# Kernel optimization log

Measured on AMD Instinct MI355X. Metric: run time of the kernel, lower is better.

Reference implementation:

```python
import jax, jax.numpy as jnp
import numpy as np

N = 131072          # total nodes per batched graph side
E = 524288          # total edges per batched graph side (avg degree 4)
B = 4096            # number of graph pairs
NPG = 32            # nodes per graph
NEG_SLOPE = 0.2
LN_EPS = 1e-5


def setup_inputs() -> dict:
    key = jax.random.key(0)
    ks = jax.random.split(key, 40)
    rn = lambda k, s, sc=0.05: jax.random.normal(k, s, dtype=jnp.float32) * sc
    inp = {}
    inp["feat1"] = jax.random.normal(ks[0], (N, 6), dtype=jnp.float32)
    inp["feat2"] = jax.random.normal(ks[1], (N, 6), dtype=jnp.float32)
    inp["llm_emb"] = jax.random.normal(ks[2], (B, 1024), dtype=jnp.float32)
    inp["src1"] = jax.random.randint(ks[3], (E,), 0, N, dtype=jnp.int32)
    inp["dst1"] = jax.random.randint(ks[4], (E,), 0, N, dtype=jnp.int32)
    inp["src2"] = jax.random.randint(ks[5], (E,), 0, N, dtype=jnp.int32)
    inp["dst2"] = jax.random.randint(ks[6], (E,), 0, N, dtype=jnp.int32)
    inp["gid"] = (jnp.arange(N, dtype=jnp.int32) // NPG).astype(jnp.int32)
    # shared GAT weights (layer: W[in,H*Dh], attn_l[H,Dh], attn_r[H,Dh], bias[H*Dh])
    inp["W1"] = rn(ks[7], (6, 128));   inp["al1"] = rn(ks[8], (4, 32));  inp["ar1"] = rn(ks[9], (4, 32));  inp["b1"] = rn(ks[10], (128,))
    inp["W2"] = rn(ks[11], (128, 128)); inp["al2"] = rn(ks[12], (4, 32)); inp["ar2"] = rn(ks[13], (4, 32)); inp["b2"] = rn(ks[14], (128,))
    inp["W3"] = rn(ks[15], (128, 256)); inp["al3"] = rn(ks[16], (4, 64)); inp["ar3"] = rn(ks[17], (4, 64)); inp["b3"] = rn(ks[18], (256,))
    # fusion
    inp["Wpg"] = rn(ks[19], (512, 512)); inp["bpg"] = rn(ks[20], (512,))
    inp["Wpl"] = rn(ks[21], (1024, 512)); inp["bpl"] = rn(ks[22], (512,))
    inp["Wv"] = rn(ks[23], (512, 512));  inp["bv"] = rn(ks[24], (512,))
    inp["Wo"] = rn(ks[25], (512, 512));  inp["bo"] = rn(ks[26], (512,))
    inp["gamma"] = jnp.ones((512,), jnp.float32); inp["beta"] = jnp.zeros((512,), jnp.float32)
    # classifier
    inp["Wc1"] = rn(ks[27], (512, 256)); inp["bc1"] = rn(ks[28], (256,))
    inp["Wc2"] = rn(ks[29], (256, 1));   inp["bc2"] = rn(ks[30], (1,))
    return inp


def _gat(x, src, dst, W, al, ar, b):
    # DGL GATConv: e_ij = LeakyReLU(a_l.h_src + a_r.h_dst), softmax over edges per dst
    H, Dh = al.shape
    h = (x @ W).reshape(-1, H, Dh)                 # [N,H,Dh]
    el = jnp.sum(h * al, axis=-1)                  # [N,H]
    er = jnp.sum(h * ar, axis=-1)                  # [N,H]
    e = jax.nn.leaky_relu(el[src] + er[dst], NEG_SLOPE)   # [E,H]
    m = jax.ops.segment_max(e, dst, num_segments=N)
    a = jnp.exp(e - m[dst])
    s = jax.ops.segment_sum(a, dst, num_segments=N)
    alpha = a / jnp.where(s[dst] == 0, 1.0, s[dst])       # [E,H]
    out = jax.ops.segment_sum(alpha[:, :, None] * h[src], dst, num_segments=N)
    return out.reshape(-1, H * Dh) + b


def _gnn(x, src, dst, gid, W1, al1, ar1, b1, W2, al2, ar2, b2, W3, al3, ar3, b3):
    h = jax.nn.relu(_gat(x, src, dst, W1, al1, ar1, b1))
    h = jax.nn.relu(_gat(h, src, dst, W2, al2, ar2, b2))
    h = _gat(h, src, dst, W3, al3, ar3, b3)        # [N,256]
    sums = jax.ops.segment_sum(h, gid, num_segments=B)
    cnt = jax.ops.segment_sum(jnp.ones((h.shape[0], 1), h.dtype), gid, num_segments=B)
    return sums / cnt                               # [B,256] mean_nodes


def reference(feat1, feat2, llm_emb, src1, dst1, src2, dst2, gid,
              W1, al1, ar1, b1, W2, al2, ar2, b2, W3, al3, ar3, b3,
              Wpg, bpg, Wpl, bpl, Wv, bv, Wo, bo, gamma, beta,
              Wc1, bc1, Wc2, bc2):
    h1 = _gnn(feat1, src1, dst1, gid, W1, al1, ar1, b1, W2, al2, ar2, b2, W3, al3, ar3, b3)
    h2 = _gnn(feat2, src2, dst2, gid, W1, al1, ar1, b1, W2, al2, ar2, b2, W3, al3, ar3, b3)
    pair = jnp.concatenate([h1, h2], axis=1)        # [B,512]
    gp = pair @ Wpg + bpg                           # [B,512]
    lp = llm_emb @ Wpl + bpl                        # [B,512]
    # MHA with kv seq_len 1: softmax over a single key == 1 -> out = W_o(W_v gp)
    attn = (gp @ Wv + bv) @ Wo + bo
    x = attn + lp
    mu = jnp.mean(x, axis=-1, keepdims=True)
    var = jnp.mean((x - mu) ** 2, axis=-1, keepdims=True)
    fused = (x - mu) / jnp.sqrt(var + LN_EPS) * gamma + beta
    hcls = jax.nn.relu(fused @ Wc1 + bc1)
    return jax.nn.sigmoid(hcls @ Wc2 + bc2)         # [B,1]
```

## Files before the change

kernel.cpp:

```cpp
#include <hip/hip_runtime.h>
#include <hip/hip_fp8.h>

#define NN 131072
#define NE 524288
#define NB 4096
#define CAP 16
#define NEG_SLOPE 0.2f
#define LN_EPS 1e-5f
#define LOG2E 1.44269504088896f

#define NBKT 1024
#define NBLK1 256
#define CELL_CAP 24

typedef unsigned short bf16;
typedef __attribute__((ext_vector_type(8))) short short8;
typedef __attribute__((ext_vector_type(4))) float floatx4;
typedef __attribute__((ext_vector_type(2))) float floatx2;

#if __has_builtin(__builtin_amdgcn_exp2f)
#define EXP2(x) __builtin_amdgcn_exp2f(x)
#else
#define EXP2(x) exp2f(x)
#endif

__device__ __forceinline__ float bf2f(bf16 h) {
    return __uint_as_float((unsigned)h << 16);
}
__device__ __forceinline__ bf16 f2bf(float f) {
    unsigned u = __float_as_uint(f);
    unsigned r = (u + 0x7FFFu + ((u >> 16) & 1u)) >> 16;
    return (bf16)r;
}
__device__ __forceinline__ unsigned pkbf(float lo, float hi) {
    unsigned r;
    asm("v_cvt_pk_bf16_f32 %0, %1, %2" : "=v"(r) : "v"(lo), "v"(hi));
    return r;
}
__device__ __forceinline__ unsigned char ftofp8(float f) {
    return (unsigned char)(__builtin_amdgcn_cvt_pk_fp8_f32(f, f, 0, false) & 0xFF);
}
__device__ __forceinline__ float leaky(float x) {
    return fmaxf(x, 0.f) + NEG_SLOPE * fminf(x, 0.f);
}

__global__ __launch_bounds__(256) void part_edges_kernel(
        const int* __restrict__ s0, const int* __restrict__ d0,
        const int* __restrict__ s1, const int* __restrict__ d1,
        unsigned* __restrict__ cells, int* __restrict__ counts) {
    __shared__ int lcnt[NBKT];
    int blk = blockIdx.x, t = threadIdx.x;
    for (int i = t; i < NBKT; i += 256) lcnt[i] = 0;
    __syncthreads();
    int side = blk >= (NBLK1 / 2);
    const int4* dp = (const int4*)(side ? d1 : d0);
    const int4* sp = (const int4*)(side ? s1 : s0);
    int base4 = (blk - side * (NBLK1 / 2)) * 1024;
    int gbase = side * NN;
#pragma unroll
    for (int it = 0; it < 4; it++) {
        int e4 = base4 + it * 256 + t;
        int4 dd = dp[e4];
        int4 ss = sp[e4];
        int d[4] = {gbase + dd.x, gbase + dd.y, gbase + dd.z, gbase + dd.w};
        int s[4] = {gbase + ss.x, gbase + ss.y, gbase + ss.z, gbase + ss.w};
#pragma unroll
        for (int k = 0; k < 4; k++) {
            int b = d[k] >> 8;
            int r = atomicAdd(&lcnt[b], 1);
            if (r < CELL_CAP)
                cells[((size_t)b * NBLK1 + blk) * CELL_CAP + r] =
                    ((unsigned)s[k] << 8) | (unsigned)(d[k] & 255);
        }
    }
    __syncthreads();
    for (int i = t; i < NBKT; i += 256) {
        int c = lcnt[i];
        counts[i * NBLK1 + blk] = (c > CELL_CAP) ? CELL_CAP : c;
    }
}

__global__ __launch_bounds__(256) void build_slots_kernel(
        const unsigned* __restrict__ cells, const int* __restrict__ counts,
        int* __restrict__ deg, int* __restrict__ slots) {
    __shared__ int ldeg[256];
    __shared__ int lslot[256 * CAP];
    int b = blockIdx.x, t = threadIdx.x;
    ldeg[t] = 0;
    for (int i = t; i < 256 * CAP; i += 256) lslot[i] = 0;
    __syncthreads();
    int cnt = counts[b * NBLK1 + t];
    const unsigned* cp = cells + ((size_t)b * NBLK1 + t) * CELL_CAP;
    for (int i = 0; i < cnt; i++) {
        unsigned v = cp[i];
        int d = v & 255;
        int s = (int)(v >> 8);
        int p = atomicAdd(&ldeg[d], 1);
        if (p < CAP) lslot[d * CAP + p] = s;
    }
    __syncthreads();
    int node0 = b * 256;
    deg[node0 + t] = ldeg[t];
    for (int i = t; i < 256 * CAP; i += 256)
        slots[(size_t)node0 * CAP + i] = lslot[i];
}

#define PREP_TOTAL (16384 + 524288 + 131072 + 2048 + 2048 + 48 + 4096 + 131072)

__global__ void prep_all_kernel(const float* __restrict__ W2, const float* __restrict__ W3,
                                const float* __restrict__ Wpl, const float* __restrict__ Wc1,
                                const float* __restrict__ W1,
                                const float* __restrict__ al1, const float* __restrict__ ar1,
                                const float* __restrict__ al2, const float* __restrict__ ar2,
                                const float* __restrict__ al3, const float* __restrict__ ar3,
                                const float* __restrict__ b1v,
                                bf16* __restrict__ W2t, bf16* __restrict__ Wplt,
                                bf16* __restrict__ Wc1t,
                                bf16* __restrict__ Ff2, bf16* __restrict__ Ff3,
                                float* __restrict__ F1, bf16* __restrict__ W1f,
                                bf16* __restrict__ W3bdt) {
    int i = blockIdx.x * blockDim.x + threadIdx.x;
    if (i < 16384) {
        int c = i >> 7, k = i & 127;
        W2t[i] = f2bf(W2[k * 128 + c]);
        return;
    }
    i -= 16384;
    if (i < 524288) {
        int c = i >> 10, k = i & 1023;
        Wplt[i] = f2bf(Wpl[k * 512 + c]);
        return;
    }
    i -= 524288;
    if (i < 131072) {
        int c = i >> 9, k = i & 511;
        Wc1t[i] = f2bf(Wc1[k * 256 + c]);
        return;
    }
    i -= 131072;
    if (i < 2048) {
        int c = i >> 7, k = i & 127;
        float s = 0.f;
        if (c < 8) {
            const float* a = (c < 4) ? al2 : ar2;
            int hh = c & 3;
            for (int d = 0; d < 32; d++) s += W2[k * 128 + hh * 32 + d] * a[hh * 32 + d];
        }
        Ff2[i] = f2bf(s);
        return;
    }
    i -= 2048;
    if (i < 2048) {
        int c = i >> 7, k = i & 127;
        float s = 0.f;
        if (c < 8) {
            const float* a = (c < 4) ? al3 : ar3;
            int hh = c & 3;
            for (int d = 0; d < 64; d++) s += W3[k * 256 + hh * 64 + d] * a[hh * 64 + d];
        }
        Ff3[i] = f2bf(s);
        return;
    }
    i -= 2048;
    if (i < 48) {
        int k = i >> 3, c = i & 7;
        const float* a = (c < 4) ? al1 : ar1;
        int hh = c & 3;
        float s = 0.f;
        for (int d = 0; d < 32; d++) s += W1[k * 128 + hh * 32 + d] * a[hh * 32 + d];
        F1[k * 8 + c] = s * LOG2E;
        return;
    }
    i -= 48;
    if (i < 4096) {
        int c = i >> 5, k = i & 31;
        int h = c >> 5, d = k & 7;
        float v = 0.f;
        if ((k >> 3) == h) {
            if (d < 6) v = W1[d * 128 + c];
            else if (d == 6) v = b1v[c];
        }
        W1f[i] = f2bf(v);
        return;
    }
    i -= 4096;
    if (i < 131072) {
        int c = i >> 9, r = i & 511;
        int hr = r >> 7, k = r & 127;
        float v = (hr == (c >> 6)) ? W3[k * 256 + c] : 0.f;
        W3bdt[i] = f2bf(v);
    }
}

__global__ void f2bf_kernel(const float* __restrict__ x, bf16* __restrict__ y) {
    int i = blockIdx.x * blockDim.x + threadIdx.x;
    float4 v = ((const float4*)x)[i];
    ushort4 u;
    u.x = f2bf(v.x); u.y = f2bf(v.y); u.z = f2bf(v.z); u.w = f2bf(v.w);
    ((ushort4*)y)[i] = u;
}

__global__ void wt_kernel(const float* __restrict__ W, bf16* __restrict__ Wt, int K, int C) {
    int i = blockIdx.x * blockDim.x + threadIdx.x;
    if (i >= K * C) return;
    int c = i / K, k = i - c * K;
    Wt[i] = f2bf(W[(size_t)k * C + c]);
}


__global__ void featelr_kernel(const float* __restrict__ f0, const float* __restrict__ f1,
                               const float* __restrict__ F1, float* __restrict__ fpk,
                               float* __restrict__ el, float* __restrict__ er) {
    int n = blockIdx.x * blockDim.x + threadIdx.x;
    const float* x = (n < NN) ? (f0 + (size_t)n * 6) : (f1 + (size_t)(n - NN) * 6);
    float xv[6];
#pragma unroll
    for (int k = 0; k < 6; k++) xv[k] = x[k];
    float4* o = (float4*)(fpk + (size_t)n * 8);
    o[0] = make_float4(xv[0], xv[1], xv[2], xv[3]);
    o[1] = make_float4(xv[4], xv[5], 0.f, 0.f);
    float4 elv, erv;
    float* ep = (float*)&elv;
    float* rp = (float*)&erv;
#pragma unroll
    for (int c = 0; c < 4; c++) {
        float sl = 0.f, sr = 0.f;
#pragma unroll
        for (int k = 0; k < 6; k++) {
            sl += xv[k] * F1[k * 8 + c];
            sr += xv[k] * F1[k * 8 + c + 4];
        }
        ep[c] = sl;
        rp[c] = sr;
    }
    *(float4*)(el + (size_t)n * 4) = elv;
    *(float4*)(er + (size_t)n * 4) = erv;
}

__global__ __launch_bounds__(256) void agg1mfma_kernel(
        const float* __restrict__ fpk, const float* __restrict__ el,
        const float* __restrict__ er, const int* __restrict__ deg,
        const int* __restrict__ slots, const bf16* __restrict__ W1fg,
        bf16* __restrict__ xb) {
    __shared__ bf16 sW[128 * 40];
    __shared__ bf16 sagg[256 * 40];
    int t = threadIdx.x;
    if (t < 128) {
        const uint4* src = (const uint4*)(W1fg + t * 32);
        uint4* dstp = (uint4*)(sW + t * 40);
        dstp[0] = src[0]; dstp[1] = src[1]; dstp[2] = src[2]; dstp[3] = src[3];
    }

    int node = blockIdx.x * 256 + t;
    int dg = deg[node];
    dg = (dg > CAP) ? CAP : dg;
    float4 er4 = *(const float4*)(er + (size_t)node * 4);
    const int* sp = slots + (size_t)node * CAP;
    float a0[4], a1[4], a2[4], a3[4], a4[4], a5[4], ss[4];
#pragma unroll
    for (int h = 0; h < 4; h++) {
        a0[h] = a1[h] = a2[h] = a3[h] = a4[h] = a5[h] = ss[h] = 0.f;
    }
    for (int p = 0; p < dg; p += 4) {
        int4 s4 = *(const int4*)(sp + p);
        int sarr[4] = {s4.x, s4.y, s4.z, s4.w};
#pragma unroll
        for (int k = 0; k < 4; k++) {
            bool vld = (p + k) < dg;
            int g = vld ? sarr[k] : s4.x;
            float4 e4 = *(const float4*)(el + (size_t)g * 4);
            float4 xa = *(const float4*)(fpk + (size_t)g * 8);
            float4 xc = *(const float4*)(fpk + (size_t)g * 8 + 4);
            float eh[4] = {e4.x, e4.y, e4.z, e4.w};
            float rh[4] = {er4.x, er4.y, er4.z, er4.w};
#pragma unroll
            for (int h = 0; h < 4; h++) {
                float z = eh[h] + rh[h];
                float w = EXP2(fmaxf(z, 0.f) + NEG_SLOPE * fminf(z, 0.f));
                w = vld ? w : 0.f;
                ss[h] += w;
                a0[h] += w * xa.x; a1[h] += w * xa.y; a2[h] += w * xa.z;
                a3[h] += w * xa.w; a4[h] += w * xc.x; a5[h] += w * xc.y;
            }
        }
    }
#pragma unroll
    for (int h = 0; h < 4; h++) {
        float rs = (dg > 0) ? 1.f / ss[h] : 0.f;
        uint4 o;
        o.x = pkbf(a0[h] * rs, a1[h] * rs);
        o.y = pkbf(a2[h] * rs, a3[h] * rs);
        o.z = pkbf(a4[h] * rs, a5[h] * rs);
        o.w = 0x00003F80u;
        *(uint4*)(sagg + t * 40 + h * 8) = o;
    }
    __syncthreads();

    int wave = t >> 6, lane = t & 63;
    int mlane = lane & 15, quad = lane >> 4;
    short8 af[8];
#pragma unroll
    for (int j = 0; j < 8; j++)
        af[j] = *(const short8*)(sW + (j * 16 + mlane) * 40 + quad * 8);
    floatx4 z4 = (floatx4){0.f, 0.f, 0.f, 0.f};
#pragma unroll
    for (int nt = 0; nt < 4; nt++) {
        int lrow = wave * 64 + nt * 16 + mlane;
        short8 bfr = *(const short8*)(sagg + lrow * 40 + quad * 8);
        floatx4 c[8];
#pragma unroll
        for (int j = 0; j < 8; j++)
            c[j] = __builtin_amdgcn_mfma_f32_16x16x32_bf16(af[j], bfr, z4, 0, 0, 0);
        bf16* op = xb + (size_t)(blockIdx.x * 256 + lrow) * 128 + quad * 4;
#pragma unroll
        for (int j = 0; j < 8; j++) {
            uint2 o;
            o.x = pkbf(fmaxf(c[j][0], 0.f), fmaxf(c[j][1], 0.f));
            o.y = pkbf(fmaxf(c[j][2], 0.f), fmaxf(c[j][3], 0.f));
            *(uint2*)(op + j * 16) = o;
        }
    }
}


__device__ __forceinline__ void softmax_phaseA(const float* __restrict__ el,
                                               const float* __restrict__ er,
                                               const int* __restrict__ slots,
                                               int wid, int dg, int lane,
                                               float* alpha_out, int* src_out) {
    int e = lane & 15, h = lane >> 4;
    int sA = slots[(size_t)wid * CAP + e];
    int sAc = (e < dg) ? sA : 0;
    float erh = er[wid * 4 + h];
    float elv = el[sAc * 4 + h];
    float w = (e < dg) ? __expf(leaky(elv + erh)) : 0.f;
    float ssum = w;
    ssum += __shfl_xor(ssum, 1, 64);
    ssum += __shfl_xor(ssum, 2, 64);
    ssum += __shfl_xor(ssum, 4, 64);
    ssum += __shfl_xor(ssum, 8, 64);
    *alpha_out = (dg > 0) ? w * (1.f / ssum) : 0.f;
    *src_out = sAc;
}

__global__ void agg2_kernel(const unsigned char* __restrict__ h8, const float* __restrict__ el,
                            const float* __restrict__ er, const int* __restrict__ deg,
                            const int* __restrict__ slots, const float* __restrict__ bias,
                            unsigned char* __restrict__ out) {
    int t = blockIdx.x * blockDim.x + threadIdx.x;
    int wid = t >> 5;
    int gl = threadIdx.x & 31;
    int dg = deg[wid];
    dg = (dg > CAP) ? CAP : dg;
    int head = gl >> 3;
    int fbase = gl * 4;
    float erh = er[wid * 4 + head];
    const int* sp = slots + (size_t)wid * CAP;
    float a0 = 0.f, a1 = 0.f, a2 = 0.f, a3 = 0.f, ssum = 0.f;

    for (int p = 0; p < dg; p += 4) {
        int4 s4 = *(const int4*)(sp + p);
        int s[4]; bool v[4];
        s[0] = s4.x; v[0] = true;
        v[1] = p + 1 < dg; s[1] = v[1] ? s4.y : s4.x;
        v[2] = p + 2 < dg; s[2] = v[2] ? s4.z : s4.x;
        v[3] = p + 3 < dg; s[3] = v[3] ? s4.w : s4.x;
        float elv[4]; unsigned u1[4];
#pragma unroll
        for (int k = 0; k < 4; k++) {
            elv[k] = el[s[k] * 4 + head];
            u1[k] = *(const unsigned*)(h8 + (size_t)s[k] * 128 + fbase);
        }
#pragma unroll
        for (int k = 0; k < 4; k++) {
            float w = v[k] ? __expf(leaky(elv[k] + erh)) : 0.f;
            ssum += w;
            floatx2 lo = __builtin_amdgcn_cvt_pk_f32_fp8((int)u1[k], false);
            floatx2 hi = __builtin_amdgcn_cvt_pk_f32_fp8((int)u1[k], true);
            a0 += w * lo[0]; a1 += w * lo[1];
            a2 += w * hi[0]; a3 += w * hi[1];
        }
    }
    float rs = (dg > 0) ? 1.f / ssum : 0.f;
    float4 bbv = *(const float4*)(bias + fbase);
    float v0 = fmaxf(a0 * rs + bbv.x, 0.f), v1 = fmaxf(a1 * rs + bbv.y, 0.f);
    float v2 = fmaxf(a2 * rs + bbv.z, 0.f), v3 = fmaxf(a3 * rs + bbv.w, 0.f);
    unsigned w8 = (unsigned)__builtin_amdgcn_cvt_pk_fp8_f32(v0, v1, 0, false);
    w8 = (unsigned)__builtin_amdgcn_cvt_pk_fp8_f32(v2, v3, (int)w8, true);
    *(unsigned*)(out + (size_t)wid * 128 + fbase) = w8;
}

__global__ __launch_bounds__(256) void elr3_kernel(const unsigned char* __restrict__ x8,
                                                   const bf16* __restrict__ Ff3,
                                                   float* __restrict__ el,
                                                   float* __restrict__ er) {
    int wave = threadIdx.x >> 6, lane = threadIdx.x & 63;
    int mlane = lane & 15, quad = lane >> 4;
    int node0 = blockIdx.x * 64 + wave * 16;
    floatx4 acc = (floatx4){0.f, 0.f, 0.f, 0.f};
#pragma unroll
    for (int kb = 0; kb < 4; kb++) {
        short8 bfr = *(const short8*)(Ff3 + mlane * 128 + kb * 32 + quad * 8);
        uint2 u8 = *(const uint2*)(x8 + (size_t)(node0 + mlane) * 128 + kb * 32 + quad * 8);
        floatx2 f01 = __builtin_amdgcn_cvt_pk_f32_fp8((int)u8.x, false);
        floatx2 f23 = __builtin_amdgcn_cvt_pk_f32_fp8((int)u8.x, true);
        floatx2 f45 = __builtin_amdgcn_cvt_pk_f32_fp8((int)u8.y, false);
        floatx2 f67 = __builtin_amdgcn_cvt_pk_f32_fp8((int)u8.y, true);
        short8 af;
        unsigned* ap = (unsigned*)&af;
        ap[0] = pkbf(f01[0], f01[1]); ap[1] = pkbf(f23[0], f23[1]);
        ap[2] = pkbf(f45[0], f45[1]); ap[3] = pkbf(f67[0], f67[1]);
        acc = __builtin_amdgcn_mfma_f32_16x16x32_bf16(af, bfr, acc, 0, 0, 0);
    }
    if (mlane < 8) {
        float* dst = (mlane < 4) ? el : er;
        int h = mlane & 3;
#pragma unroll
        for (int r = 0; r < 4; r++) {
            int node = node0 + quad * 4 + r;
            dst[node * 4 + h] = acc[r];
        }
    }
}

__global__ void agg3pool_kernel(const unsigned char* __restrict__ x8,
                                const float* __restrict__ el, const float* __restrict__ er,
                                const int* __restrict__ deg, const int* __restrict__ slots,
                                bf16* __restrict__ poolagg) {
    __shared__ float red[4][4][128];
    __shared__ float salpha[4][136][4];
    __shared__ int   ssrc[4][136];
    int side = blockIdx.x >> 12;
    int b = blockIdx.x & 4095;
    int nodebase = side * NN + b * 32;
    int grp = threadIdx.x >> 6, lane = threadIdx.x & 63;
    int e = lane & 15, h = lane >> 4;
    int esl = lane >> 5;
    int ch4 = (lane & 31) * 4;

    int off = 0;
    for (int nn = 0; nn < 8; nn++) {
        int wid = nodebase + grp * 8 + nn;
        int dg = deg[wid];
        dg = (dg > CAP) ? CAP : dg;
        float alpha; int sAc;
        softmax_phaseA(el, er, slots, wid, dg, lane, &alpha, &sAc);
        if (e < dg) {
            salpha[grp][off + e][h] = alpha;
            if (h == 0) ssrc[grp][off + e] = sAc;
        }
        off += dg;
    }
    int padded = (off + 7) & ~7;
    if (lane < padded - off) {
        int j = off + lane;
        *(float4*)&salpha[grp][j][0] = make_float4(0.f, 0.f, 0.f, 0.f);
        ssrc[grp][j] = 0;
    }

    floatx2 acc[4][2];
#pragma unroll
    for (int hh = 0; hh < 4; hh++) {
        acc[hh][0] = (floatx2){0.f, 0.f};
        acc[hh][1] = (floatx2){0.f, 0.f};
    }
    for (int j = 0; j < padded; j += 8) {
        int sc[4]; float4 av[4]; unsigned u[4];
#pragma unroll
        for (int k = 0; k < 4; k++) {
            int je = j + 2 * k + esl;
            sc[k] = ssrc[grp][je];
            av[k] = *(const float4*)&salpha[grp][je][0];
        }
#pragma unroll
        for (int k = 0; k < 4; k++)
            u[k] = *(const unsigned*)(x8 + (size_t)sc[k] * 128 + ch4);
#pragma unroll
        for (int k = 0; k < 4; k++) {
            floatx2 lo = __builtin_amdgcn_cvt_pk_f32_fp8((int)u[k], false);
            floatx2 hi = __builtin_amdgcn_cvt_pk_f32_fp8((int)u[k], true);
            float aa[4] = {av[k].x, av[k].y, av[k].z, av[k].w};
#pragma unroll
            for (int hh = 0; hh < 4; hh++) {
                floatx2 a2 = (floatx2){aa[hh], aa[hh]};
                acc[hh][0] += a2 * lo;
                acc[hh][1] += a2 * hi;
            }
        }
    }
#pragma unroll
    for (int hh = 0; hh < 4; hh++)
#pragma unroll
        for (int jj = 0; jj < 2; jj++) {
            acc[hh][jj][0] += __shfl_xor(acc[hh][jj][0], 32, 64);
            acc[hh][jj][1] += __shfl_xor(acc[hh][jj][1], 32, 64);
        }
    if (lane < 32) {
#pragma unroll
        for (int hh = 0; hh < 4; hh++)
            *(float4*)&red[grp][hh][ch4] =
                make_float4(acc[hh][0][0], acc[hh][0][1], acc[hh][1][0], acc[hh][1][1]);
    }
    __syncthreads();
    int t = threadIdx.x;
    int hlo = t >> 7, c = t & 127;
    float s0 = 0.f, s1 = 0.f;
#pragma unroll
    for (int g = 0; g < 4; g++) {
        s0 += red[g][hlo][c];
        s1 += red[g][2 + hlo][c];
    }
    const float inv = 1.0f / 32.0f;
    size_t gbase = (size_t)(b * 2 + side) * 512;
    poolagg[gbase + t] = f2bf(s0 * inv);
    poolagg[gbase + t + 256] = f2bf(s1 * inv);
}

template <bool FOLD, bool OUT8, bool PAIR>
__global__ __launch_bounds__(256) void mgemm_kernel(const bf16* __restrict__ A,
                                                    const bf16* __restrict__ Wt,
                                                    const float* __restrict__ bias,
                                                    void* __restrict__ out,
                                                    int K, int C, int relu,
                                                    const bf16* __restrict__ Ff,
                                                    float* __restrict__ el,
                                                    float* __restrict__ er) {
    __shared__ short As[128 * 48];
    __shared__ short Bs[128 * 48];
    int t = threadIdx.x;
    int wave = t >> 6, lane = t & 63;
    int wm = (wave >> 1) * 64, wn = (wave & 1) * 64;
    int bm = blockIdx.x * 128, bn = blockIdx.y * 128;
    int m_lane = lane & 15, quad = lane >> 4;
    bool dofold = FOLD && (blockIdx.y == 0) && (wn == 0);

    floatx4 acc[4][4];
#pragma unroll
    for (int i = 0; i < 4; i++)
#pragma unroll
        for (int j = 0; j < 4; j++) acc[i][j] = (floatx4){0.f, 0.f, 0.f, 0.f};
    floatx4 facc[4];
    if (FOLD) {
#pragma unroll
        for (int i = 0; i < 4; i++) facc[i] = (floatx4){0.f, 0.f, 0.f, 0.f};
    }

    int lrow = t >> 2, lq = t & 3;
    for (int k0 = 0; k0 < K; k0 += 32) {
        __syncthreads();
#pragma unroll
        for (int pass = 0; pass < 2; pass++) {
            int row = lrow + pass * 64;
            *(short8*)&As[row * 48 + lq * 8] =
                *(const short8*)(A + (size_t)(bm + row) * K + k0 + lq * 8);
            *(short8*)&Bs[row * 48 + lq * 8] =
                *(const short8*)(Wt + (size_t)(bn + row) * K + k0 + lq * 8);
        }
        __syncthreads();
        short8 af[4], bf[4];
#pragma unroll
        for (int i = 0; i < 4; i++)
            af[i] = *(const short8*)&As[(wm + i * 16 + m_lane) * 48 + quad * 8];
#pragma unroll
        for (int j = 0; j < 4; j++)
            bf[j] = *(const short8*)&Bs[(wn + j * 16 + m_lane) * 48 + quad * 8];
        if (dofold) {
            short8 fbv = *(const short8*)(Ff + m_lane * K + k0 + quad * 8);
#pragma unroll
            for (int i = 0; i < 4; i++)
                facc[i] = __builtin_amdgcn_mfma_f32_16x16x32_bf16(af[i], fbv, facc[i], 0, 0, 0);
        }
#pragma unroll
        for (int i = 0; i < 4; i++)
#pragma unroll
            for (int j = 0; j < 4; j++)
                acc[i][j] = __builtin_amdgcn_mfma_f32_16x16x32_bf16(af[i], bf[j], acc[i][j], 0, 0, 0);
    }

#pragma unroll
    for (int i = 0; i < 4; i++) {
#pragma unroll
        for (int j = 0; j < 4; j++) {
            int gc = bn + wn + j * 16 + m_lane;
            float bbv = bias ? bias[gc] : 0.f;
#pragma unroll
            for (int r = 0; r < 4; r++) {
                int gr = bm + wm + i * 16 + quad * 4 + r;
                float v = acc[i][j][r] + bbv;
                if (relu) v = fmaxf(v, 0.f);
                if (OUT8)      ((unsigned char*)out)[(size_t)gr * C + gc] = ftofp8(v);
                else if (PAIR) ((bf16*)out)[(size_t)(gr >> 1) * 512 + (gr & 1) * 256 + gc] = f2bf(v);
                else           ((bf16*)out)[(size_t)gr * C + gc] = f2bf(v);
            }
        }
    }
    if (dofold && m_lane < 8) {
        float* dst = (m_lane < 4) ? el : er;
        int hh = m_lane & 3;
#pragma unroll
        for (int i = 0; i < 4; i++)
#pragma unroll
            for (int r = 0; r < 4; r++) {
                int gr = bm + wm + i * 16 + quad * 4 + r;
                dst[gr * 4 + hh] = facc[i][r];
            }
    }
}

__global__ __launch_bounds__(256) void fgemm512_kernel(const float* __restrict__ A,
                                                       const float* __restrict__ B,
                                                       float* __restrict__ C) {
    const int BK = 16;
    __shared__ float As[BK][68];
    __shared__ float Bs[BK][68];
    int t = threadIdx.x;
    int bm = blockIdx.x * 64, bn = blockIdx.y * 64;
    int tm0 = (t & 15) * 4, tn0 = (t >> 4) * 4;
    float acc[4][4] = {};
    int la_m = t >> 2, la_k = (t & 3) * 4;
    int lb_k = t >> 4, lb_c = (t & 15) * 4;

    for (int k0 = 0; k0 < 512; k0 += BK) {
        float4 a4 = *(const float4*)(A + (size_t)(bm + la_m) * 512 + k0 + la_k);
        float4 b4 = *(const float4*)(B + (size_t)(k0 + lb_k) * 512 + bn + lb_c);
        As[la_k + 0][la_m] = a4.x; As[la_k + 1][la_m] = a4.y;
        As[la_k + 2][la_m] = a4.z; As[la_k + 3][la_m] = a4.w;
        *(float4*)&Bs[lb_k][lb_c] = b4;
        __syncthreads();
#pragma unroll
        for (int k = 0; k < BK; k++) {
            float4 av = *(const float4*)&As[k][tm0];
            float4 bv = *(const float4*)&Bs[k][tn0];
            acc[0][0] += av.x * bv.x; acc[0][1] += av.x * bv.y; acc[0][2] += av.x * bv.z; acc[0][3] += av.x * bv.w;
            acc[1][0] += av.y * bv.x; acc[1][1] += av.y * bv.y; acc[1][2] += av.y * bv.z; acc[1][3] += av.y * bv.w;
            acc[2][0] += av.z * bv.x; acc[2][1] += av.z * bv.y; acc[2][2] += av.z * bv.z; acc[2][3] += av.z * bv.w;
            acc[3][0] += av.w * bv.x; acc[3][1] += av.w * bv.y; acc[3][2] += av.w * bv.z; acc[3][3] += av.w * bv.w;
        }
        __syncthreads();
    }
#pragma unroll
    for (int i = 0; i < 4; i++) {
        float4 o = make_float4(acc[i][0], acc[i][1], acc[i][2], acc[i][3]);
        *(float4*)(C + (size_t)(bm + tm0 + i) * 512 + bn + tn0) = o;
    }
}

__global__ void biasstep_kernel(const float* __restrict__ vin, const float* __restrict__ M,
                                const float* __restrict__ badd, float* __restrict__ vout) {
    int c = blockIdx.x * blockDim.x + threadIdx.x;
    float s = 0.f;
    for (int k = 0; k < 512; k++) s += vin[k] * M[(size_t)k * 512 + c];
    vout[c] = s + badd[c];
}


__global__ void ln_kernel(const bf16* __restrict__ attn, const bf16* __restrict__ lp,
                          const float* __restrict__ gamma, const float* __restrict__ beta,
                          bf16* __restrict__ out) {
    __shared__ float red[256];
    int b = blockIdx.x, t = threadIdx.x;
    size_t base = (size_t)b * 512;
    float x0 = bf2f(attn[base + t]) + bf2f(lp[base + t]);
    float x1 = bf2f(attn[base + 256 + t]) + bf2f(lp[base + 256 + t]);
    red[t] = x0 + x1; __syncthreads();
    for (int off = 128; off > 0; off >>= 1) { if (t < off) red[t] += red[t + off]; __syncthreads(); }
    float mu = red[0] * (1.0f / 512.0f);
    __syncthreads();
    float d0 = x0 - mu, d1 = x1 - mu;
    red[t] = d0 * d0 + d1 * d1; __syncthreads();
    for (int off = 128; off > 0; off >>= 1) { if (t < off) red[t] += red[t + off]; __syncthreads(); }
    float rstd = rsqrtf(red[0] * (1.0f / 512.0f) + LN_EPS);
    out[base + t]       = f2bf(d0 * rstd * gamma[t] + beta[t]);
    out[base + 256 + t] = f2bf(d1 * rstd * gamma[256 + t] + beta[256 + t]);
}

__global__ void cls2_kernel(const bf16* __restrict__ hc, const float* __restrict__ Wc2,
                            const float* __restrict__ bc2, float* __restrict__ out) {
    int wid = (blockIdx.x * blockDim.x + threadIdx.x) >> 6;
    int lane = threadIdx.x & 63;
    if (wid >= NB) return;
    float s = 0.f;
#pragma unroll
    for (int j = 0; j < 4; j++) {
        int k = lane + 64 * j;
        s += bf2f(hc[(size_t)wid * 256 + k]) * Wc2[k];
    }
    for (int off = 32; off > 0; off >>= 1) s += __shfl_down(s, off);
    if (lane == 0) {
        float v = s + bc2[0];
        out[wid] = 1.0f / (1.0f + __expf(-v));
    }
}


static inline size_t alup(size_t x) { return (x + 255) & ~(size_t)255; }

extern "C" void kernel_launch(void* const* d_in, const int* in_sizes, int n_in,
                              void* d_out, int out_size, void* d_ws, size_t ws_size,
                              hipStream_t stream) {
    const float* feat0 = (const float*)d_in[0];
    const float* feat1 = (const float*)d_in[1];
    const float* llm = (const float*)d_in[2];
    const int* srcs[2] = {(const int*)d_in[3], (const int*)d_in[5]};
    const int* dsts[2] = {(const int*)d_in[4], (const int*)d_in[6]};
    const float* W1 = (const float*)d_in[8];
    const float* al[3] = {(const float*)d_in[9],  (const float*)d_in[13], (const float*)d_in[17]};
    const float* ar[3] = {(const float*)d_in[10], (const float*)d_in[14], (const float*)d_in[18]};
    const float* bb[3] = {(const float*)d_in[11], (const float*)d_in[15], (const float*)d_in[19]};
    const float* W2 = (const float*)d_in[12];
    const float* W3 = (const float*)d_in[16];
    const float* Wpg = (const float*)d_in[20]; const float* bpg = (const float*)d_in[21];
    const float* Wpl = (const float*)d_in[22]; const float* bpl = (const float*)d_in[23];
    const float* Wv  = (const float*)d_in[24]; const float* bv  = (const float*)d_in[25];
    const float* Wo  = (const float*)d_in[26]; const float* bo  = (const float*)d_in[27];
    const float* gamma = (const float*)d_in[28]; const float* beta = (const float*)d_in[29];
    const float* Wc1 = (const float*)d_in[30]; const float* bc1 = (const float*)d_in[31];
    const float* Wc2 = (const float*)d_in[32]; const float* bc2 = (const float*)d_in[33];
    float* outp = (float*)d_out;

    const size_t N2 = (size_t)2 * NN;

    char* p = (char*)d_ws;
    auto take = [&](size_t bytes) { char* r = p; p += alup(bytes); return r; };
    bf16*  xb     = (bf16*)take(N2 * 128 * 2);
    char*  regB   = (char*)take(N2 * 256);
    float* el     = (float*)take(N2 * 4 * 4);
    float* er     = (float*)take(N2 * 4 * 4);
    int*   deg    = (int*)take(N2 * 4);
    int*   slots  = (int*)take(N2 * CAP * 4);
    bf16*  pair   = (bf16*)take((size_t)NB * 512 * 2);
    bf16*  llm_bf = (bf16*)take((size_t)NB * 1024 * 2);
    bf16*  W2t  = (bf16*)take(128 * 128 * 2);
    bf16*  Wplt = (bf16*)take(1024 * 512 * 2);
    bf16*  Wc1t = (bf16*)take(512 * 256 * 2);
    bf16*  Wcot = (bf16*)take(512 * 512 * 2);
    bf16*  W3bdt = (bf16*)take(256 * 512 * 2);
    float* F1   = (float*)take(6 * 8 * 4);
    bf16*  Ff2  = (bf16*)take(16 * 128 * 2);
    bf16*  Ff3  = (bf16*)take(16 * 128 * 2);
    bf16*  W1fg = (bf16*)take(128 * 32 * 2);
    float* c1   = (float*)take(512 * 512 * 4);
    float* c2   = (float*)take(512 * 512 * 4);
    float* bias1 = (float*)take(512 * 4);
    float* bco   = (float*)take(512 * 4);
    unsigned char* x8 = (unsigned char*)xb;
    unsigned* cells = (unsigned*)regB;
    int* counts = (int*)(regB + (size_t)NBKT * NBLK1 * CELL_CAP * 4);
    float* fpk          = (float*)regB;
    unsigned char* hb2  = (unsigned char*)regB;
    bf16* poolagg = (bf16*)(regB + 32 * 1024 * 1024);
    bf16* fbb   = (bf16*)regB;
    bf16* lp    = fbb + (size_t)0 * NB * 512;
    bf16* attn  = fbb + (size_t)1 * NB * 512;
    bf16* fused = fbb + (size_t)2 * NB * 512;
    bf16* hc    = fbb + (size_t)3 * NB * 512;
    (void)ws_size; (void)n_in; (void)in_sizes; (void)out_size;

    auto mgemm = [&](const bf16* A, const bf16* Wt, const float* bias, bf16* o,
                     int M, int K, int C, int relu) {
        dim3 g(M / 128, C / 128);
        mgemm_kernel<false, false, false><<<g, 256, 0, stream>>>(A, Wt, bias, o, K, C, relu,
                                                                 nullptr, nullptr, nullptr);
    };

    part_edges_kernel<<<NBLK1, 256, 0, stream>>>(srcs[0], dsts[0], srcs[1], dsts[1],
                                                 cells, counts);
    build_slots_kernel<<<NBKT, 256, 0, stream>>>(cells, counts, deg, slots);

    prep_all_kernel<<<(PREP_TOTAL + 255) / 256, 256, 0, stream>>>(
        W2, W3, Wpl, Wc1, W1, al[0], ar[0], al[1], ar[1], al[2], ar[2], bb[0],
        W2t, Wplt, Wc1t, Ff2, Ff3, F1, W1fg, W3bdt);
    f2bf_kernel<<<NB * 1024 / 4 / 256, 256, 0, stream>>>(llm, llm_bf);
    {
        dim3 g8(8, 8);
        fgemm512_kernel<<<g8, 256, 0, stream>>>(Wpg, Wv, c1);
        fgemm512_kernel<<<g8, 256, 0, stream>>>(c1, Wo, c2);
        wt_kernel<<<(512 * 512 + 255) / 256, 256, 0, stream>>>(c2, Wcot, 512, 512);
        biasstep_kernel<<<2, 256, 0, stream>>>(bpg, Wv, bv, bias1);
        biasstep_kernel<<<2, 256, 0, stream>>>(bias1, Wo, bo, bco);
    }

    featelr_kernel<<<2 * NN / 256, 256, 0, stream>>>(feat0, feat1, F1, fpk, el, er);
    agg1mfma_kernel<<<2 * NN / 256, 256, 0, stream>>>(fpk, el, er, deg, slots, W1fg, xb);
    {
        dim3 g(2 * NN / 128, 1);
        mgemm_kernel<true, true, false><<<g, 256, 0, stream>>>(xb, W2t, nullptr, hb2,
                                                               128, 128, 0, Ff2, el, er);
    }
    agg2_kernel<<<2 * NN * 32 / 256, 256, 0, stream>>>(hb2, el, er, deg, slots, bb[1], x8);
    elr3_kernel<<<2 * NN / 64, 256, 0, stream>>>(x8, Ff3, el, er);
    agg3pool_kernel<<<2 * NB, 256, 0, stream>>>(x8, el, er, deg, slots, poolagg);
    {
        dim3 g(8192 / 128, 256 / 128);
        mgemm_kernel<false, false, true><<<g, 256, 0, stream>>>(poolagg, W3bdt, bb[2], pair,
                                                                512, 256, 0,
                                                                nullptr, nullptr, nullptr);
    }

    mgemm(llm_bf, Wplt, bpl, lp, NB, 1024, 512, 0);
    mgemm(pair, Wcot, bco, attn, NB, 512, 512, 0);
    ln_kernel<<<NB, 256, 0, stream>>>(attn, lp, gamma, beta, fused);
    mgemm(fused, Wc1t, bc1, hc, NB, 512, 256, 1);
    cls2_kernel<<<NB / 4, 256, 0, stream>>>(hc, Wc2, bc2, outp);
}
```

Baseline: 555.7 us.

## Store layer-1 features and attention logits in bf16; widen edge partition grid

Layer-1 node features and the el/er attention logits are now stored as packed bf16 instead of fp32. This halves the bytes gathered per edge in the first aggregation kernel. The edge partition kernel now launches four times as many blocks, each handling one int4 per thread, with smaller per-cell capacity, so more work runs in parallel. The slot builder loops over the larger number of cells per bucket. The change risks bf16 precision loss in the attention logits and overflow drops when a cell gets more than 12 edges.

```diff
diff --git a/kernel.cpp b/kernel.cpp
--- a/kernel.cpp
+++ b/kernel.cpp
@@ -10,8 +10,8 @@
 #define LOG2E 1.44269504088896f
 
 #define NBKT 1024
-#define NBLK1 256
-#define CELL_CAP 24
+#define NBLK1 1024
+#define CELL_CAP 12
 
 typedef unsigned short bf16;
 typedef __attribute__((ext_vector_type(8))) short short8;
@@ -31,6 +31,12 @@
     unsigned u = __float_as_uint(f);
     unsigned r = (u + 0x7FFFu + ((u >> 16) & 1u)) >> 16;
     return (bf16)r;
+}
+__device__ __forceinline__ floatx2 upk2(unsigned u) {
+    floatx2 r;
+    r[0] = __uint_as_float(u << 16);
+    r[1] = __uint_as_float(u & 0xFFFF0000u);
+    return r;
 }
 __device__ __forceinline__ unsigned pkbf(float lo, float hi) {
     unsigned r;
@@ -55,23 +61,19 @@
     int side = blk >= (NBLK1 / 2);
     const int4* dp = (const int4*)(side ? d1 : d0);
     const int4* sp = (const int4*)(side ? s1 : s0);
-    int base4 = (blk - side * (NBLK1 / 2)) * 1024;
+    int e4 = (blk - side * (NBLK1 / 2)) * 256 + t;
     int gbase = side * NN;
-#pragma unroll
-    for (int it = 0; it < 4; it++) {
-        int e4 = base4 + it * 256 + t;
-        int4 dd = dp[e4];
-        int4 ss = sp[e4];
-        int d[4] = {gbase + dd.x, gbase + dd.y, gbase + dd.z, gbase + dd.w};
-        int s[4] = {gbase + ss.x, gbase + ss.y, gbase + ss.z, gbase + ss.w};
-#pragma unroll
-        for (int k = 0; k < 4; k++) {
-            int b = d[k] >> 8;
-            int r = atomicAdd(&lcnt[b], 1);
-            if (r < CELL_CAP)
-                cells[((size_t)b * NBLK1 + blk) * CELL_CAP + r] =
-                    ((unsigned)s[k] << 8) | (unsigned)(d[k] & 255);
-        }
+    int4 dd = dp[e4];
+    int4 ss = sp[e4];
+    int d[4] = {gbase + dd.x, gbase + dd.y, gbase + dd.z, gbase + dd.w};
+    int s[4] = {gbase + ss.x, gbase + ss.y, gbase + ss.z, gbase + ss.w};
+#pragma unroll
+    for (int k = 0; k < 4; k++) {
+        int b = d[k] >> 8;
+        int r = atomicAdd(&lcnt[b], 1);
+        if (r < CELL_CAP)
+            cells[((size_t)b * NBLK1 + blk) * CELL_CAP + r] =
+                ((unsigned)s[k] << 8) | (unsigned)(d[k] & 255);
     }
     __syncthreads();
     for (int i = t; i < NBKT; i += 256) {
@@ -89,14 +91,16 @@
     ldeg[t] = 0;
     for (int i = t; i < 256 * CAP; i += 256) lslot[i] = 0;
     __syncthreads();
-    int cnt = counts[b * NBLK1 + t];
-    const unsigned* cp = cells + ((size_t)b * NBLK1 + t) * CELL_CAP;
-    for (int i = 0; i < cnt; i++) {
-        unsigned v = cp[i];
-        int d = v & 255;
-        int s = (int)(v >> 8);
-        int p = atomicAdd(&ldeg[d], 1);
-        if (p < CAP) lslot[d * CAP + p] = s;
+    for (int cc = t; cc < NBLK1; cc += 256) {
+        int cnt = counts[b * NBLK1 + cc];
+        const unsigned* cp = cells + ((size_t)b * NBLK1 + cc) * CELL_CAP;
+        for (int i = 0; i < cnt; i++) {
+            unsigned v = cp[i];
+            int d = v & 255;
+            int s = (int)(v >> 8);
+            int p = atomicAdd(&ldeg[d], 1);
+            if (p < CAP) lslot[d * CAP + p] = s;
+        }
     }
     __syncthreads();
     int node0 = b * 256;
@@ -209,19 +213,20 @@
 
 
 __global__ void featelr_kernel(const float* __restrict__ f0, const float* __restrict__ f1,
-                               const float* __restrict__ F1, float* __restrict__ fpk,
-                               float* __restrict__ el, float* __restrict__ er) {
+                               const float* __restrict__ F1, bf16* __restrict__ fpk,
+                               bf16* __restrict__ el1, bf16* __restrict__ er1) {
     int n = blockIdx.x * blockDim.x + threadIdx.x;
     const float* x = (n < NN) ? (f0 + (size_t)n * 6) : (f1 + (size_t)(n - NN) * 6);
     float xv[6];
 #pragma unroll
     for (int k = 0; k < 6; k++) xv[k] = x[k];
-    float4* o = (float4*)(fpk + (size_t)n * 8);
-    o[0] = make_float4(xv[0], xv[1], xv[2], xv[3]);
-    o[1] = make_float4(xv[4], xv[5], 0.f, 0.f);
-    float4 elv, erv;
-    float* ep = (float*)&elv;
-    float* rp = (float*)&erv;
+    uint4 o;
+    o.x = pkbf(xv[0], xv[1]);
+    o.y = pkbf(xv[2], xv[3]);
+    o.z = pkbf(xv[4], xv[5]);
+    o.w = 0u;
+    *(uint4*)(fpk + (size_t)n * 8) = o;
+    float ep[4], rp[4];
 #pragma unroll
     for (int c = 0; c < 4; c++) {
         float sl = 0.f, sr = 0.f;
@@ -233,13 +238,16 @@
         ep[c] = sl;
         rp[c] = sr;
     }
-    *(float4*)(el + (size_t)n * 4) = elv;
-    *(float4*)(er + (size_t)n * 4) = erv;
+    uint2 eo, ro;
+    eo.x = pkbf(ep[0], ep[1]); eo.y = pkbf(ep[2], ep[3]);
+    ro.x = pkbf(rp[0], rp[1]); ro.y = pkbf(rp[2], rp[3]);
+    *(uint2*)(el1 + (size_t)n * 4) = eo;
+    *(uint2*)(er1 + (size_t)n * 4) = ro;
 }
 
 __global__ __launch_bounds__(256) void agg1mfma_kernel(
-        const float* __restrict__ fpk, const float* __restrict__ el,
-        const float* __restrict__ er, const int* __restrict__ deg,
+        const bf16* __restrict__ fpk, const bf16* __restrict__ el1,
+        const bf16* __restrict__ er1, const int* __restrict__ deg,
         const int* __restrict__ slots, const bf16* __restrict__ W1fg,
         bf16* __restrict__ xb) {
     __shared__ bf16 sW[128 * 40];
@@ -254,7 +262,9 @@
     int node = blockIdx.x * 256 + t;
     int dg = deg[node];
     dg = (dg > CAP) ? CAP : dg;
-    float4 er4 = *(const float4*)(er + (size_t)node * 4);
+    uint2 eru = *(const uint2*)(er1 + (size_t)node * 4);
+    floatx2 r01 = upk2(eru.x), r23 = upk2(eru.y);
+    float rh[4] = {r01[0], r01[1], r23[0], r23[1]};
     const int* sp = slots + (size_t)node * CAP;
     float a0[4], a1[4], a2[4], a3[4], a4[4], a5[4], ss[4];
 #pragma unroll
@@ -268,19 +278,19 @@
         for (int k = 0; k < 4; k++) {
             bool vld = (p + k) < dg;
             int g = vld ? sarr[k] : s4.x;
-            float4 e4 = *(const float4*)(el + (size_t)g * 4);
-            float4 xa = *(const float4*)(fpk + (size_t)g * 8);
-            float4 xc = *(const float4*)(fpk + (size_t)g * 8 + 4);
-            float eh[4] = {e4.x, e4.y, e4.z, e4.w};
-            float rh[4] = {er4.x, er4.y, er4.z, er4.w};
+            uint2 eu = *(const uint2*)(el1 + (size_t)g * 4);
+            uint4 xu = *(const uint4*)(fpk + (size_t)g * 8);
+            floatx2 e01 = upk2(eu.x), e23 = upk2(eu.y);
+            floatx2 x01 = upk2(xu.x), x23 = upk2(xu.y), x45 = upk2(xu.z);
+            float eh[4] = {e01[0], e01[1], e23[0], e23[1]};
 #pragma unroll
             for (int h = 0; h < 4; h++) {
                 float z = eh[h] + rh[h];
                 float w = EXP2(fmaxf(z, 0.f) + NEG_SLOPE * fminf(z, 0.f));
                 w = vld ? w : 0.f;
                 ss[h] += w;
-                a0[h] += w * xa.x; a1[h] += w * xa.y; a2[h] += w * xa.z;
-                a3[h] += w * xa.w; a4[h] += w * xc.x; a5[h] += w * xc.y;
+                a0[h] += w * x01[0]; a1[h] += w * x01[1]; a2[h] += w * x23[0];
+                a3[h] += w * x23[1]; a4[h] += w * x45[0]; a5[h] += w * x45[1];
             }
         }
     }
@@ -744,9 +754,11 @@
     float* bias1 = (float*)take(512 * 4);
     float* bco   = (float*)take(512 * 4);
     unsigned char* x8 = (unsigned char*)xb;
+    bf16* el1 = (bf16*)el;
+    bf16* er1 = (bf16*)er;
     unsigned* cells = (unsigned*)regB;
     int* counts = (int*)(regB + (size_t)NBKT * NBLK1 * CELL_CAP * 4);
-    float* fpk          = (float*)regB;
+    bf16* fpk           = (bf16*)regB;
     unsigned char* hb2  = (unsigned char*)regB;
     bf16* poolagg = (bf16*)(regB + 32 * 1024 * 1024);
     bf16* fbb   = (bf16*)regB;
@@ -780,8 +792,8 @@
         biasstep_kernel<<<2, 256, 0, stream>>>(bias1, Wo, bo, bco);
     }
 
-    featelr_kernel<<<2 * NN / 256, 256, 0, stream>>>(feat0, feat1, F1, fpk, el, er);
-    agg1mfma_kernel<<<2 * NN / 256, 256, 0, stream>>>(fpk, el, er, deg, slots, W1fg, xb);
+    featelr_kernel<<<2 * NN / 256, 256, 0, stream>>>(feat0, feat1, F1, fpk, el1, er1);
+    agg1mfma_kernel<<<2 * NN / 256, 256, 0, stream>>>(fpk, el1, er1, deg, slots, W1fg, xb);
     {
         dim3 g(2 * NN / 128, 1);
         mgemm_kernel<true, true, false><<<g, 256, 0, stream>>>(xb, W2t, nullptr, hb2,
```

Result: no change. 548.6 us (-1.3%).
